# Kernel optimization log

Measured on AMD Instinct MI355X. Metric: run time of the kernel, lower is better.

## Reference

```python
import jax, jax.numpy as jnp
import numpy as np

H, HKV, D, HID, T = 16, 4, 128, 2048, 4096
THETA = 10000.0
EPS = 1e-5
NEG = -1e30


def setup_inputs() -> dict:
    key = jax.random.key(0)
    ks = jax.random.split(key, 4)
    return {
        "positions": jnp.arange(T, dtype=jnp.int32),
        "hidden_states": jax.random.normal(ks[0], (T, HID), jnp.float32),
        "w_qkv": jax.random.normal(ks[1], ((H + 2 * HKV) * D, HID), jnp.float32) * 0.02,
        "w_o": jax.random.normal(ks[2], (HID, H * D), jnp.float32) * 0.02,
        "q_norm_w": jnp.ones((H * D,), jnp.float32),
        "k_norm_w": jnp.ones((HKV * D,), jnp.float32),
    }


def _rope(pos, x):
    # x: [T, nh, D]; neox-style rotary over full head_dim
    half = D // 2
    inv_freq = 1.0 / (THETA ** (jnp.arange(0, D, 2, dtype=jnp.float32) / D))  # [D/2]
    ang = pos.astype(jnp.float32)[:, None] * inv_freq  # [T, D/2]
    cos = jnp.cos(ang)[:, None, :]
    sin = jnp.sin(ang)[:, None, :]
    x1, x2 = x[..., :half], x[..., half:]
    return jnp.concatenate([x1 * cos - x2 * sin, x2 * cos + x1 * sin], axis=-1)


def _rmsnorm(x, w):
    var = jnp.mean(x * x, axis=-1, keepdims=True)
    return x * jax.lax.rsqrt(var + EPS) * w


def reference(positions, hidden_states, w_qkv, w_o, q_norm_w, k_norm_w):
    qkv = hidden_states @ w_qkv.T  # [T, (H+2*HKV)*D]
    q, k, v = jnp.split(qkv, [H * D, H * D + HKV * D], axis=-1)
    # RoPE per head
    q = _rope(positions, q.reshape(T, H, D)).reshape(T, H * D)
    k = _rope(positions, k.reshape(T, HKV, D)).reshape(T, HKV * D)
    # QK-norm over the flattened (all-heads) q_size / kv_size, as in the module
    q = _rmsnorm(q, q_norm_w)
    k = _rmsnorm(k, k_norm_w)
    qh = q.reshape(T, H, D)
    kh = jnp.repeat(k.reshape(T, HKV, D), H // HKV, axis=1)  # GQA expand
    vh = jnp.repeat(v.reshape(T, HKV, D), H // HKV, axis=1)
    scores = jnp.einsum('qhd,khd->hqk', qh, kh) * (D ** -0.5)  # [H, T, T]
    causal = jnp.tril(jnp.ones((T, T), dtype=bool))
    scores = jnp.where(causal, scores, NEG)
    p = jax.nn.softmax(scores, axis=-1)
    attn = jnp.einsum('hqk,khd->qhd', p, vh).reshape(T, H * D)
    return attn @ w_o.T  # [T, HID]
```

## Files before the change

### kernel.cpp

```cpp
#include <hip/hip_runtime.h>
#include <hip/hip_bf16.h>

#define T_SEQ 4096
#define HID   2048
#define NH    16
#define NKV   4
#define HD    128
#define QKV_N 3072
#define QSCALE 0.12751744f
#define SMAX 24.0f

typedef unsigned short u16;
typedef __bf16 bf16x8 __attribute__((ext_vector_type(8)));
typedef float floatx4 __attribute__((ext_vector_type(4)));
typedef float floatx16 __attribute__((ext_vector_type(16)));

__device__ __forceinline__ float b2f(u16 u) {
  union { unsigned int i; float f; } x; x.i = ((unsigned int)u) << 16; return x.f;
}
__device__ __forceinline__ u16 f2b(float f) {
  union { float f; unsigned int i; } x; x.f = f;
  unsigned int i = x.i;
  unsigned int r = (i + 0x7FFFu + ((i >> 16) & 1u)) >> 16;
  return (u16)r;
}
__device__ __forceinline__ void gload_lds16(const u16* g, u16* lds) {
  __builtin_amdgcn_global_load_lds(
      (const __attribute__((address_space(1))) unsigned int*)g,
      (__attribute__((address_space(3))) unsigned int*)lds, 16, 0, 0);
}

__global__ __launch_bounds__(256) void conv_f32_bf16(const float* __restrict__ src,
                                                     u16* __restrict__ dst, int n8) {
  int i = blockIdx.x * 256 + threadIdx.x;
  if (i >= n8) return;
  const float4* s = (const float4*)(src + (size_t)i * 8);
  float4 a = s[0], b = s[1];
  union { u16 h[8]; uint4 u; } r;
  r.h[0] = f2b(a.x); r.h[1] = f2b(a.y); r.h[2] = f2b(a.z); r.h[3] = f2b(a.w);
  r.h[4] = f2b(b.x); r.h[5] = f2b(b.y); r.h[6] = f2b(b.z); r.h[7] = f2b(b.w);
  *(uint4*)(dst + (size_t)i * 8) = r.u;
}

template <int CF>
__global__ __launch_bounds__(256) void gemm_bt(const u16* __restrict__ A, int lda,
                                               const u16* __restrict__ B, int ldb,
                                               void* __restrict__ Cv, int ldc, int K) {
  __shared__ __align__(16) u16 sA[128 * 32];
  __shared__ __align__(16) u16 sB[128 * 32];
  const int tid = threadIdx.x;
  const int wave = tid >> 6, lane = tid & 63;
  const int row0 = blockIdx.y * 128, col0 = blockIdx.x * 128;
  const int wm = (wave >> 1) * 64, wn = (wave & 1) * 64;
  const int frow = lane & 15, fk = (lane >> 4) * 8;

  floatx4 acc[4][4];
#pragma unroll
  for (int i = 0; i < 4; i++)
#pragma unroll
    for (int j = 0; j < 4; j++) acc[i][j] = (floatx4){0.f, 0.f, 0.f, 0.f};

  const int c0 = wave * 2;
  const int v0 = c0 * 64 + lane;
  const int v1 = v0 + 64;
  const u16* gA0 = A + (size_t)(row0 + (v0 >> 2)) * lda + (v0 & 3) * 8;
  const u16* gA1 = A + (size_t)(row0 + (v1 >> 2)) * lda + (v1 & 3) * 8;
  const u16* gB0 = B + (size_t)(col0 + (v0 >> 2)) * ldb + (v0 & 3) * 8;
  const u16* gB1 = B + (size_t)(col0 + (v1 >> 2)) * ldb + (v1 & 3) * 8;

  for (int k0 = 0; k0 < K; k0 += 32) {
    gload_lds16(gA0 + k0, sA + c0 * 512);
    gload_lds16(gA1 + k0, sA + c0 * 512 + 512);
    gload_lds16(gB0 + k0, sB + c0 * 512);
    gload_lds16(gB1 + k0, sB + c0 * 512 + 512);
    __syncthreads();
    bf16x8 af[4], bfv[4];
#pragma unroll
    for (int i = 0; i < 4; i++) {
      af[i]  = *(const bf16x8*)(sA + (wm + i * 16 + frow) * 32 + fk);
      bfv[i] = *(const bf16x8*)(sB + (wn + i * 16 + frow) * 32 + fk);
    }
#pragma unroll
    for (int i = 0; i < 4; i++)
#pragma unroll
      for (int j = 0; j < 4; j++)
        acc[i][j] = __builtin_amdgcn_mfma_f32_16x16x32_bf16(af[i], bfv[j], acc[i][j], 0, 0, 0);
    __syncthreads();
  }
  const int crow = (lane >> 4) * 4, ccol = lane & 15;
#pragma unroll
  for (int i = 0; i < 4; i++)
#pragma unroll
    for (int j = 0; j < 4; j++)
#pragma unroll
      for (int r = 0; r < 4; r++) {
        int rr = row0 + wm + i * 16 + crow + r;
        int cc = col0 + wn + j * 16 + ccol;
        if (CF) ((float*)Cv)[(size_t)rr * ldc + cc] = acc[i][j][r];
        else    ((u16*)Cv)[(size_t)rr * ldc + cc] = f2b(acc[i][j][r]);
      }
}

__device__ __forceinline__ void fast_sincos(float ang, float* s, float* c) {
  float r = ang * 0.15915494309189535f;
  r -= floorf(r);
  *s = __builtin_amdgcn_sinf(r);
  *c = __builtin_amdgcn_cosf(r);
}

__global__ __launch_bounds__(256) void rope_norm(const int* __restrict__ pos_arr,
                                                 u16* __restrict__ qkv,
                                                 const float* __restrict__ qnw,
                                                 const float* __restrict__ knw) {
  const int t = blockIdx.x;
  const int tid = threadIdx.x;
  const int lane = tid & 63, wave = tid >> 6;
  u16* row = qkv + (size_t)t * QKV_N;
  const float pos = (float)pos_arr[t];

  float qv[8];
  float ssq = 0.f;
#pragma unroll
  for (int i = 0; i < 8; i++) {
    int e = tid * 8 + i;
    int r = e & 127, ih = e & 63;
    float invf = exp2f(-(float)ih * 0.20762050593046015f);
    float ang = pos * invf;
    float s, c;
    fast_sincos(ang, &s, &c);
    float val;
    if (r < 64) val = b2f(row[e]) * c - b2f(row[e + 64]) * s;
    else        val = b2f(row[e]) * c + b2f(row[e - 64]) * s;
    qv[i] = val;
    ssq += val * val;
  }
  float kv[2];
  float ssk = 0.f;
  const u16* krow = row + HID;
#pragma unroll
  for (int i = 0; i < 2; i++) {
    int e = tid * 2 + i;
    int r = e & 127, ih = e & 63;
    float invf = exp2f(-(float)ih * 0.20762050593046015f);
    float ang = pos * invf;
    float s, c;
    fast_sincos(ang, &s, &c);
    float val;
    if (r < 64) val = b2f(krow[e]) * c - b2f(krow[e + 64]) * s;
    else        val = b2f(krow[e]) * c + b2f(krow[e - 64]) * s;
    kv[i] = val;
    ssk += val * val;
  }
#pragma unroll
  for (int off = 1; off < 64; off <<= 1) {
    ssq += __shfl_xor(ssq, off);
    ssk += __shfl_xor(ssk, off);
  }
  __shared__ float rq[4], rk[4];
  if (lane == 0) { rq[wave] = ssq; rk[wave] = ssk; }
  __syncthreads();
  float sq = rq[0] + rq[1] + rq[2] + rq[3];
  float sk = rk[0] + rk[1] + rk[2] + rk[3];
  float qsc = rsqrtf(sq * (1.0f / 2048.0f) + 1e-5f) * QSCALE;
  float ksc = rsqrtf(sk * (1.0f / 512.0f) + 1e-5f);
#pragma unroll
  for (int i = 0; i < 8; i++) {
    int e = tid * 8 + i;
    row[e] = f2b(qv[i] * qsc * qnw[e]);
  }
#pragma unroll
  for (int i = 0; i < 2; i++) {
    int e = tid * 2 + i;
    row[HID + e] = f2b(kv[i] * ksc * knw[e]);
  }
}

__global__ __launch_bounds__(256) void transpose_v(const u16* __restrict__ qkv,
                                                   u16* __restrict__ vt) {
  __shared__ __align__(16) u16 tile[64][136];
  const int tid = threadIdx.x;
  const int h = blockIdx.y;
  const int t0 = blockIdx.x * 64;
#pragma unroll
  for (int p = 0; p < 4; p++) {
    int v = p * 256 + tid;
    int r = v >> 4, c = v & 15;
    const u16* g = qkv + (size_t)(t0 + r) * QKV_N + (HID + NKV * HD) + h * HD + c * 8;
    *(uint4*)(&tile[r][c * 8]) = *(const uint4*)g;
  }
  __syncthreads();
#pragma unroll
  for (int p = 0; p < 4; p++) {
    int v = p * 256 + tid;
    int d = v >> 3, c8 = v & 7;
    union { u16 s[8]; uint4 q; } tmp;
#pragma unroll
    for (int i = 0; i < 8; i++) tmp.s[i] = tile[c8 * 8 + i][d];
    u16* g = vt + ((size_t)h * HD + d) * T_SEQ + t0 + c8 * 8;
    *(uint4*)g = tmp.q;
  }
}

__device__ __forceinline__ void stage_kv(const u16* __restrict__ kbase,
                                         const u16* __restrict__ vbase, int kv0,
                                         u16* sk, u16* sv, int tid) {
  const int w = tid >> 6, lane = tid & 63;
#pragma unroll
  for (int i = 0; i < 4; i++) {
    int c = w * 256 + i * 64 + lane;
    int kv = c >> 4, ch = c & 15;
    const u16* g = kbase + (size_t)(kv0 + kv) * QKV_N + ((ch ^ (kv & 7)) * 8);
    gload_lds16(g, sk + (size_t)(w * 256 + i * 64) * 8);
  }
#pragma unroll
  for (int i = 0; i < 4; i++) {
    int c = w * 256 + i * 64 + lane;
    int d = c >> 3, c2 = c & 7;
    const u16* g = vbase + (size_t)d * T_SEQ + kv0 + ((c2 ^ (d & 7)) * 8);
    gload_lds16(g, sv + (size_t)(w * 256 + i * 64) * 8);
  }
}

__global__ __launch_bounds__(256, 2) void attn_kernel(u16* __restrict__ qkv,
                                                      const u16* __restrict__ vt) {
  __shared__ __align__(16) u16 sK[2][64 * 128];
  __shared__ __align__(16) u16 sV[2][128 * 64];
  const int tid = threadIdx.x;
  const int wave = tid >> 6, lane = tid & 63;
  const int bid = blockIdx.x;
  int qt, h;
  if (bid < 256) { qt = bid >> 3; h = bid & 7; }
  else           { qt = 31 - ((bid & 255) >> 3); h = 8 + (bid & 7); }
  const int kvh = h >> 2;
  const int ql = lane & 31;
  const int fq2 = lane >> 5;
  const u16* kbase = qkv + HID + (size_t)kvh * HD;
  const u16* vbase = vt + (size_t)kvh * HD * T_SEQ;

  const int qb = qt * 128;
  const int qw = qb + wave * 32;
  const int qmax = qw + 31;
  const int qrow = qw + ql;
  bf16x8 qf[8];
  const u16* qp = qkv + (size_t)qrow * QKV_N + h * HD + fq2 * 8;
#pragma unroll
  for (int kc = 0; kc < 8; kc++) qf[kc] = *(const bf16x8*)(qp + kc * 16);
  floatx16 O[4];
#pragma unroll
  for (int dt = 0; dt < 4; dt++)
#pragma unroll
    for (int r = 0; r < 16; r++) O[dt][r] = 0.f;
  float l_part = 0.f;

  const int nst = 2 * (qt + 1);
  stage_kv(kbase, vbase, 0, sK[0], sV[0], tid);
#pragma unroll 1
  for (int s = 0; s < nst; s++) {
    __syncthreads();
    if (s + 1 < nst)
      stage_kv(kbase, vbase, (s + 1) * 64, sK[(s + 1) & 1], sV[(s + 1) & 1], tid);
    const int kv0 = s * 64;
    if (kv0 <= qmax) {
      const u16* sk = sK[s & 1];
      const u16* sv = sV[s & 1];
      const int ntv = (kv0 + 32 <= qmax) ? 2 : 1;
#pragma unroll
      for (int nt = 0; nt < 2; nt++) {
        if (nt < ntv) {
          floatx16 S;
#pragma unroll
          for (int r = 0; r < 16; r++) S[r] = -SMAX;
          __builtin_amdgcn_s_setprio(1);
#pragma unroll
          for (int kc = 0; kc < 8; kc++) {
            int ch = (kc * 2 + fq2) ^ (ql & 7);
            bf16x8 kf = *(const bf16x8*)(sk + ((nt * 32 + ql) * 16 + ch) * 8);
            S = __builtin_amdgcn_mfma_f32_32x32x16_bf16(kf, qf[kc], S, 0, 0, 0);
          }
          __builtin_amdgcn_s_setprio(0);
          const bool tmask = (kv0 + nt * 32 + 31) > qw;
#pragma unroll
          for (int r = 0; r < 16; r++) {
            float v = S[r];
            if (tmask) {
              int kvg = kv0 + nt * 32 + (r & 3) + ((r >> 2) << 3) + (fq2 << 2);
              v = (kvg > qrow) ? -1e30f : v;
            }
            float p = __builtin_amdgcn_exp2f(v);
            l_part += p;
            S[r] = p;
          }
          unsigned cp[8];
#pragma unroll
          for (int i = 0; i < 8; i++) {
            unsigned wv;
            asm("v_cvt_pk_bf16_f32 %0, %1, %2"
                : "=v"(wv) : "v"(S[i * 2]), "v"(S[i * 2 + 1]));
            cp[i] = wv;
          }
          union { unsigned u[4]; bf16x8 v; } pf0, pf1;
          {
            auto r0 = __builtin_amdgcn_permlane32_swap(cp[0], cp[2], false, false);
            pf0.u[0] = r0[0]; pf0.u[2] = r0[1];
            auto r1 = __builtin_amdgcn_permlane32_swap(cp[1], cp[3], false, false);
            pf0.u[1] = r1[0]; pf0.u[3] = r1[1];
            auto r2 = __builtin_amdgcn_permlane32_swap(cp[4], cp[6], false, false);
            pf1.u[0] = r2[0]; pf1.u[2] = r2[1];
            auto r3 = __builtin_amdgcn_permlane32_swap(cp[5], cp[7], false, false);
            pf1.u[1] = r3[0]; pf1.u[3] = r3[1];
          }
          __builtin_amdgcn_s_setprio(1);
#pragma unroll
          for (int c = 0; c < 2; c++) {
            bf16x8 pf = c ? pf1.v : pf0.v;
#pragma unroll
            for (int dt = 0; dt < 4; dt++) {
              int ch2 = ((nt * 2 + c) * 2 + fq2) ^ (ql & 7);
              bf16x8 vf = *(const bf16x8*)(sv + ((dt * 32 + ql) * 8 + ch2) * 8);
              O[dt] = __builtin_amdgcn_mfma_f32_32x32x16_bf16(vf, pf, O[dt], 0, 0, 0);
            }
          }
          __builtin_amdgcn_s_setprio(0);
        }
      }
    }
  }
  float l = l_part + __shfl_xor(l_part, 32);
  float inv = 1.0f / fmaxf(l, 1e-30f);
  u16* orow = qkv + (size_t)qrow * QKV_N + h * HD;
#pragma unroll
  for (int dt = 0; dt < 4; dt++)
#pragma unroll
    for (int rg = 0; rg < 4; rg++) {
      union { u16 hh[4]; uint2 uu; } wv;
#pragma unroll
      for (int rr = 0; rr < 4; rr++) wv.hh[rr] = f2b(O[dt][rg * 4 + rr] * inv);
      *(uint2*)(orow + dt * 32 + rg * 8 + fq2 * 4) = wv.uu;
    }
}

extern "C" void kernel_launch(void* const* d_in, const int* in_sizes, int n_in,
                              void* d_out, int out_size, void* d_ws, size_t ws_size,
                              hipStream_t stream) {
  const int* positions = (const int*)d_in[0];
  const float* hidden = (const float*)d_in[1];
  const float* w_qkv = (const float*)d_in[2];
  const float* w_o = (const float*)d_in[3];
  const float* qnw = (const float*)d_in[4];
  const float* knw = (const float*)d_in[5];
  float* out = (float*)d_out;

  u16* qkv  = (u16*)d_ws;
  u16* bufA = qkv + (size_t)T_SEQ * QKV_N;
  u16* bufB = bufA + (size_t)T_SEQ * HID;

  conv_f32_bf16<<<4096, 256, 0, stream>>>(hidden, bufA, T_SEQ * HID / 8);
  conv_f32_bf16<<<3072, 256, 0, stream>>>(w_qkv, bufB, QKV_N * HID / 8);
  gemm_bt<0><<<dim3(QKV_N / 128, T_SEQ / 128), 256, 0, stream>>>(
      bufA, HID, bufB, HID, qkv, QKV_N, HID);
  rope_norm<<<T_SEQ, 256, 0, stream>>>(positions, qkv, qnw, knw);
  conv_f32_bf16<<<2048, 256, 0, stream>>>(w_o, bufA, HID * HID / 8);
  transpose_v<<<dim3(T_SEQ / 64, NKV), 256, 0, stream>>>(qkv, bufB);
  attn_kernel<<<512, 256, 0, stream>>>(qkv, bufB);
  gemm_bt<1><<<dim3(HID / 128, T_SEQ / 128), 256, 0, stream>>>(
      qkv, QKV_N, bufA, HID, out, HID, HID);
}
```

Measured before the change: 412.2 us.

## Split long causal attention tiles across two blocks with atomic combine

The query tiles in the upper half of the sequence have the most causal KV work, so each is now split into two KV halves handled by separate blocks. The schedule is rearranged to interleave split and unsplit tiles. Partial outputs and row sums are accumulated with float atomics into scratch placed in the output buffer, and a new combine kernel normalizes them and writes bf16. This targets load imbalance and tail effects, at the cost of extra memsets, atomic traffic and one more launch.

```diff
diff --git a/kernel.cpp b/kernel.cpp
--- a/kernel.cpp
+++ b/kernel.cpp
@@ -222,23 +222,39 @@
 }
 
 __global__ __launch_bounds__(256, 2) void attn_kernel(u16* __restrict__ qkv,
-                                                      const u16* __restrict__ vt) {
+                                                      const u16* __restrict__ vt,
+                                                      float* __restrict__ scratch,
+                                                      float* __restrict__ lbuf) {
   __shared__ __align__(16) u16 sK[2][64 * 128];
   __shared__ __align__(16) u16 sV[2][128 * 64];
   const int tid = threadIdx.x;
   const int wave = tid >> 6, lane = tid & 63;
   const int bid = blockIdx.x;
-  int qt, h;
-  if (bid < 256) { qt = bid >> 3; h = bid & 7; }
-  else           { qt = 31 - ((bid & 255) >> 3); h = 8 + (bid & 7); }
+
+  const int x = bid & 7, slot = bid >> 3;
+  int h, qt, part = 0;
+  bool split;
+  if (slot < 80) {
+    const int pr = slot / 10, r = slot - pr * 10;
+    if (r < 4)      { qt = 31 - 2 * pr; part = r & 1;       h = 2 * x + (r >> 1);       split = true;  }
+    else if (r < 6) { qt = 15 - pr;                         h = 2 * x + (r - 4);        split = false; }
+    else            { qt = 30 - 2 * pr; part = (r - 6) & 1; h = 2 * x + ((r - 6) >> 1); split = true;  }
+  } else {
+    const int j = slot - 80;
+    qt = 7 - (j >> 1);
+    h = 2 * x + (j & 1);
+    split = false;
+  }
+  const int s_begin = (split && part) ? (qt + 1) : 0;
+  const int s_end   = split ? (part ? 2 * (qt + 1) : (qt + 1)) : 2 * (qt + 1);
+
   const int kvh = h >> 2;
   const int ql = lane & 31;
   const int fq2 = lane >> 5;
   const u16* kbase = qkv + HID + (size_t)kvh * HD;
   const u16* vbase = vt + (size_t)kvh * HD * T_SEQ;
 
-  const int qb = qt * 128;
-  const int qw = qb + wave * 32;
+  const int qw = qt * 128 + wave * 32;
   const int qmax = qw + 31;
   const int qrow = qw + ql;
   bf16x8 qf[8];
@@ -252,17 +268,18 @@
     for (int r = 0; r < 16; r++) O[dt][r] = 0.f;
   float l_part = 0.f;
 
-  const int nst = 2 * (qt + 1);
-  stage_kv(kbase, vbase, 0, sK[0], sV[0], tid);
+  const int nsteps = s_end - s_begin;
+  stage_kv(kbase, vbase, s_begin * 64, sK[0], sV[0], tid);
 #pragma unroll 1
-  for (int s = 0; s < nst; s++) {
+  for (int st = 0; st < nsteps; st++) {
+    const int s = s_begin + st;
     __syncthreads();
-    if (s + 1 < nst)
-      stage_kv(kbase, vbase, (s + 1) * 64, sK[(s + 1) & 1], sV[(s + 1) & 1], tid);
+    if (st + 1 < nsteps)
+      stage_kv(kbase, vbase, (s + 1) * 64, sK[(st + 1) & 1], sV[(st + 1) & 1], tid);
     const int kv0 = s * 64;
     if (kv0 <= qmax) {
-      const u16* sk = sK[s & 1];
-      const u16* sv = sV[s & 1];
+      const u16* sk = sK[st & 1];
+      const u16* sv = sV[st & 1];
       const int ntv = (kv0 + 32 <= qmax) ? 2 : 1;
 #pragma unroll
       for (int nt = 0; nt < 2; nt++) {
@@ -326,17 +343,53 @@
     }
   }
   float l = l_part + __shfl_xor(l_part, 32);
-  float inv = 1.0f / fmaxf(l, 1e-30f);
-  u16* orow = qkv + (size_t)qrow * QKV_N + h * HD;
-#pragma unroll
-  for (int dt = 0; dt < 4; dt++)
-#pragma unroll
-    for (int rg = 0; rg < 4; rg++) {
-      union { u16 hh[4]; uint2 uu; } wv;
-#pragma unroll
-      for (int rr = 0; rr < 4; rr++) wv.hh[rr] = f2b(O[dt][rg * 4 + rr] * inv);
-      *(uint2*)(orow + dt * 32 + rg * 8 + fq2 * 4) = wv.uu;
-    }
+  if (!split) {
+    float inv = 1.0f / fmaxf(l, 1e-30f);
+    u16* orow = qkv + (size_t)qrow * QKV_N + h * HD;
+#pragma unroll
+    for (int dt = 0; dt < 4; dt++)
+#pragma unroll
+      for (int rg = 0; rg < 4; rg++) {
+        union { u16 hh[4]; uint2 uu; } wv;
+#pragma unroll
+        for (int rr = 0; rr < 4; rr++) wv.hh[rr] = f2b(O[dt][rg * 4 + rr] * inv);
+        *(uint2*)(orow + dt * 32 + rg * 8 + fq2 * 4) = wv.uu;
+      }
+  } else {
+    const int tile = h * 16 + (qt - 16);
+    float* obase = scratch + (size_t)tile * 16384 + (size_t)(wave * 32 + ql) * 128;
+#pragma unroll
+    for (int dt = 0; dt < 4; dt++)
+#pragma unroll
+      for (int rg = 0; rg < 4; rg++)
+#pragma unroll
+        for (int rr = 0; rr < 4; rr++)
+          atomicAdd(obase + dt * 32 + rg * 8 + fq2 * 4 + rr, O[dt][rg * 4 + rr]);
+    if (fq2 == 0) atomicAdd(lbuf + tile * 128 + wave * 32 + ql, l);
+  }
+}
+
+__global__ __launch_bounds__(256) void combine_split(const float* __restrict__ scratch,
+                                                     const float* __restrict__ lbuf,
+                                                     u16* __restrict__ qkv) {
+  const int t = blockIdx.x;
+  const int h = t >> 4, qt = 16 + (t & 15);
+  const int tid = threadIdx.x;
+  const int rsub = tid >> 4;
+  const int d0 = (tid & 15) * 8;
+#pragma unroll
+  for (int p = 0; p < 8; p++) {
+    int r = p * 16 + rsub;
+    float inv = 1.0f / fmaxf(lbuf[t * 128 + r], 1e-30f);
+    const float4* s4 = (const float4*)(scratch + (size_t)t * 16384 + (size_t)r * 128 + d0);
+    float4 a = s4[0], b = s4[1];
+    union { u16 hh[8]; uint4 u; } wv;
+    wv.hh[0] = f2b(a.x * inv); wv.hh[1] = f2b(a.y * inv);
+    wv.hh[2] = f2b(a.z * inv); wv.hh[3] = f2b(a.w * inv);
+    wv.hh[4] = f2b(b.x * inv); wv.hh[5] = f2b(b.y * inv);
+    wv.hh[6] = f2b(b.z * inv); wv.hh[7] = f2b(b.w * inv);
+    *(uint4*)(qkv + (size_t)(qt * 128 + r) * QKV_N + h * HD + d0) = wv.u;
+  }
 }
 
 extern "C" void kernel_launch(void* const* d_in, const int* in_sizes, int n_in,
@@ -353,6 +406,8 @@
   u16* qkv  = (u16*)d_ws;
   u16* bufA = qkv + (size_t)T_SEQ * QKV_N;
   u16* bufB = bufA + (size_t)T_SEQ * HID;
+  float* lbuf = (float*)(bufB + 2097152);
+  float* scratch = out;
 
   conv_f32_bf16<<<4096, 256, 0, stream>>>(hidden, bufA, T_SEQ * HID / 8);
   conv_f32_bf16<<<3072, 256, 0, stream>>>(w_qkv, bufB, QKV_N * HID / 8);
@@ -361,7 +416,10 @@
   rope_norm<<<T_SEQ, 256, 0, stream>>>(positions, qkv, qnw, knw);
   conv_f32_bf16<<<2048, 256, 0, stream>>>(w_o, bufA, HID * HID / 8);
   transpose_v<<<dim3(T_SEQ / 64, NKV), 256, 0, stream>>>(qkv, bufB);
-  attn_kernel<<<512, 256, 0, stream>>>(qkv, bufB);
+  hipMemsetAsync(scratch, 0, (size_t)256 * 16384 * 4, stream);
+  hipMemsetAsync(lbuf, 0, (size_t)256 * 128 * 4, stream);
+  attn_kernel<<<768, 256, 0, stream>>>(qkv, bufB, scratch, lbuf);
+  combine_split<<<256, 256, 0, stream>>>(scratch, lbuf, qkv);
   gemm_bt<1><<<dim3(HID / 128, T_SEQ / 128), 256, 0, stream>>>(
       qkv, QKV_N, bufA, HID, out, HID, HID);
 }
```

Result: slower. 559.3 us (+35.7%).
